# Performance work log

Hardware: AMD Instinct MI355X
Metric: run time of the kernel (lower is better)

Reference implementation:

```python
import jax, jax.numpy as jnp
import numpy as np

D_MODEL = 1024
N_HEADS = 16
D_K = D_MODEL // N_HEADS
B, T = 4, 2048


def setup_inputs() -> dict:
    key = jax.random.key(0)
    ks = jax.random.split(key, 6)
    scale = 1.0 / np.sqrt(D_MODEL)
    q = jax.random.normal(ks[0], (B, T, D_MODEL), dtype=jnp.float32)
    # causal mask: True = masked / ignored (upper triangle)
    causal = jnp.triu(jnp.ones((T, T), dtype=bool), k=1)
    mask = jnp.broadcast_to(causal, (B, 1, T, T))
    Wq = jax.random.normal(ks[1], (D_MODEL, D_MODEL), dtype=jnp.float32) * scale
    Wk = jax.random.normal(ks[2], (D_MODEL, D_MODEL), dtype=jnp.float32) * scale
    Wv = jax.random.normal(ks[3], (D_MODEL, D_MODEL), dtype=jnp.float32) * scale
    Wo = jax.random.normal(ks[4], (D_MODEL, D_MODEL), dtype=jnp.float32) * scale
    bq = jnp.zeros((D_MODEL,), jnp.float32)
    bk = jnp.zeros((D_MODEL,), jnp.float32)
    bv = jnp.zeros((D_MODEL,), jnp.float32)
    bo = jnp.zeros((D_MODEL,), jnp.float32)
    return {"q": q, "mask": mask, "Wq": Wq, "bq": bq, "Wk": Wk, "bk": bk,
            "Wv": Wv, "bv": bv, "Wo": Wo, "bo": bo}


def reference(q, mask, Wq, bq, Wk, bk, Wv, bv, Wo, bo):
    # Self-attention: k = v = q (module defaults). Weights stored torch-style
    # (out, in): y = x @ W.T + b.
    b, tq, _ = q.shape
    qh = (q @ Wq.T + bq).reshape(b, tq, N_HEADS, D_K).transpose(0, 2, 1, 3)  # (B,H,T,dk)
    kh = (q @ Wk.T + bk).reshape(b, tq, N_HEADS, D_K).transpose(0, 2, 1, 3)
    vh = (q @ Wv.T + bv).reshape(b, tq, N_HEADS, D_K).transpose(0, 2, 1, 3)
    attn = jnp.einsum('bhqd,bhkd->bhqk', qh, kh) / np.sqrt(D_K).astype(np.float32)
    attn = jnp.where(mask, -jnp.inf, attn)
    attn = jax.nn.softmax(attn, axis=-1)
    out = jnp.einsum('bhqk,bhkd->bhqd', attn, vh)
    out = out.transpose(0, 2, 1, 3).reshape(b, tq, D_MODEL)
    return out @ Wo.T + bo
```

## Files before the change

### kernel.cpp

```cpp
#include <hip/hip_runtime.h>
#include <hip/hip_bf16.h>
#include <stdint.h>

#define D_MODEL 1024
#define NH      16
#define DKH     64
#define BATCH   4
#define SEQ     2048
#define MROWS   (BATCH*SEQ)

typedef __hip_bfloat16 bf16;
typedef __attribute__((ext_vector_type(8))) short  bf16x8;
typedef __attribute__((ext_vector_type(4))) short  bf16x4;
typedef __attribute__((ext_vector_type(4))) float  f32x4;
typedef __attribute__((ext_vector_type(2))) unsigned int u32x2;

#define CEXP 0.18033688011112042f

__device__ __forceinline__ bf16 f2bf(float x){ return __float2bfloat16(x); }

__device__ __forceinline__ void gload_lds16(const void* g, void* l) {
  __builtin_amdgcn_global_load_lds(
      (const __attribute__((address_space(1))) unsigned int*)g,
      (__attribute__((address_space(3))) unsigned int*)l, 16, 0, 0);
}

__device__ __forceinline__ unsigned int cvtpk(float lo, float hi) {
  unsigned int r;
  asm("v_cvt_pk_bf16_f32 %0, %1, %2" : "=v"(r) : "v"(lo), "v"(hi));
  return r;
}

__global__ __launch_bounds__(256)
void cvt_all(const float* __restrict__ q,
             const float* __restrict__ w0, const float* __restrict__ w1,
             const float* __restrict__ w2, const float* __restrict__ w3,
             bf16* __restrict__ qdst, bf16* __restrict__ wdst)
{
  const int NQB = (MROWS * D_MODEL) / 1024;
  const int bid = blockIdx.x;
  const float* src;
  bf16* dst;
  int i;
  if (bid < NQB) {
    src = q; dst = qdst;
    i = bid * 1024 + threadIdx.x * 4;
  } else {
    const int b2 = bid - NQB;
    const int w = b2 >> 10;
    src = (w == 0) ? w0 : (w == 1) ? w1 : (w == 2) ? w2 : w3;
    dst = wdst + (size_t)w * (D_MODEL * D_MODEL);
    i = (b2 & 1023) * 1024 + threadIdx.x * 4;
  }
  f32x4 v = *(const f32x4*)&src[i];
  union { bf16 e[4]; bf16x4 v4; } u;
  u.e[0] = f2bf(v[0]); u.e[1] = f2bf(v[1]);
  u.e[2] = f2bf(v[2]); u.e[3] = f2bf(v[3]);
  *(bf16x4*)&dst[i] = u.v4;
}

template <int MODE>
__global__ __launch_bounds__(512, 2)
void gemm8(const bf16* __restrict__ A, const bf16* __restrict__ W,
           const float* __restrict__ b0, const float* __restrict__ b1,
           const float* __restrict__ b2, void* __restrict__ Cbase)
{
  constexpr int K    = D_MODEL;
  constexpr int NT   = K / 64;
  constexpr int SLOT = (128 + 256) * 64;
  __shared__ __align__(16) short ring[3 * SLOT];

  const int tid  = threadIdx.x;
  const int lane = tid & 63;
  const int wave = tid >> 6;
  const int lm   = lane & 15;
  const int quad = lane >> 4;
  const int wm   = (wave >> 2) * 64;
  const int wn   = (wave & 3) * 64;
  const int bm   = blockIdx.x * 128;
  const int bn   = blockIdx.y * 256;

  const int rr    = tid >> 3;
  const int kperm = ((tid & 7) ^ (rr & 7)) * 8;
  const bf16* aS0 = A + (int64_t)(bm + rr) * K + kperm;
  const bf16* aS1 = aS0 + (int64_t)64 * K;
  const bf16* bS0 = W + (int64_t)(bn + rr) * K + kperm;
  const bf16* bS1 = bS0 + (int64_t)64 * K;
  const bf16* bS2 = bS0 + (int64_t)128 * K;
  const bf16* bS3 = bS0 + (int64_t)192 * K;

  f32x4 acc[4][4] = {};

#define STAGE8(T, S)                                                          \
  do {                                                                        \
    const int k0_ = (T) * 64;                                                 \
    short* As_ = &ring[(S) * SLOT];                                           \
    short* Bs_ = As_ + 128 * 64;                                              \
    gload_lds16(aS0 + k0_, &As_[tid * 8]);                                    \
    gload_lds16(aS1 + k0_, &As_[(tid + 512) * 8]);                            \
    gload_lds16(bS0 + k0_, &Bs_[tid * 8]);                                    \
    gload_lds16(bS1 + k0_, &Bs_[(tid + 512) * 8]);                            \
    gload_lds16(bS2 + k0_, &Bs_[(tid + 1024) * 8]);                           \
    gload_lds16(bS3 + k0_, &Bs_[(tid + 1536) * 8]);                           \
  } while (0)

  STAGE8(0, 0);
  STAGE8(1, 1);

#pragma unroll
  for (int t = 0; t < NT; ++t) {
    if (t < NT - 1) asm volatile("s_waitcnt vmcnt(6)" ::: "memory");
    else            asm volatile("s_waitcnt vmcnt(0)" ::: "memory");
    __builtin_amdgcn_s_barrier();
    asm volatile("" ::: "memory");

    const short* As = &ring[(t % 3) * SLOT];
    const short* Bs = As + 128 * 64;
    short* Ad = &ring[((t + 2) % 3) * SLOT];
    short* Bd = Ad + 128 * 64;
    const bool dost = (t + 2 < NT);
    const int k2 = (t + 2) * 64;

#pragma unroll
    for (int kk = 0; kk < 2; ++kk) {
      bf16x8 af[4], bfr[4];
#pragma unroll
      for (int i = 0; i < 4; ++i) {
        const int ra = wm + i * 16 + lm;
        af[i]  = *(const bf16x8*)&As[ra * 64 + (((kk * 4 + quad) ^ (ra & 7))) * 8];
        const int rb = wn + i * 16 + lm;
        bfr[i] = *(const bf16x8*)&Bs[rb * 64 + (((kk * 4 + quad) ^ (rb & 7))) * 8];
      }
      if (dost) {
        if (kk == 0) {
          gload_lds16(aS0 + k2, &Ad[tid * 8]);
          gload_lds16(aS1 + k2, &Ad[(tid + 512) * 8]);
          gload_lds16(bS0 + k2, &Bd[tid * 8]);
        } else {
          gload_lds16(bS1 + k2, &Bd[(tid + 512) * 8]);
          gload_lds16(bS2 + k2, &Bd[(tid + 1024) * 8]);
          gload_lds16(bS3 + k2, &Bd[(tid + 1536) * 8]);
        }
      }
      __builtin_amdgcn_s_barrier();
      asm volatile("s_waitcnt lgkmcnt(0)" ::: "memory");
      __builtin_amdgcn_sched_barrier(0);
      __builtin_amdgcn_s_setprio(1);
#pragma unroll
      for (int i = 0; i < 4; ++i)
#pragma unroll
        for (int j = 0; j < 4; ++j)
          acc[i][j] = __builtin_amdgcn_mfma_f32_16x16x32_bf16(af[i], bfr[j], acc[i][j], 0, 0, 0);
      __builtin_amdgcn_s_setprio(0);
    }
  }
#undef STAGE8

  if constexpr (MODE == 1) {
    float* Cp = (float*)Cbase;
#pragma unroll
    for (int j = 0; j < 4; ++j) {
      const int n = bn + wn + j * 16 + lm;
      const float bv = b0[n];
#pragma unroll
      for (int i = 0; i < 4; ++i)
#pragma unroll
        for (int r = 0; r < 4; ++r) {
          const int m = bm + wm + i * 16 + quad * 4 + r;
          Cp[(int64_t)m * D_MODEL + n] = acc[i][j][r] + bv;
        }
    }
  } else {
    const int proj = bn >> 10;
    const int nl0  = bn & 1023;
    const float* bias = (proj == 0) ? b0 : (proj == 1) ? b1 : b2;
    if (proj == 2) {
      bf16* Vt = (bf16*)Cbase + 2 * (size_t)MROWS * D_MODEL;
#pragma unroll
      for (int j = 0; j < 4; ++j) {
        const int nl = nl0 + wn + j * 16 + lm;
        const float bv = bias[nl];
#pragma unroll
        for (int i = 0; i < 4; ++i) {
          const int m0 = bm + wm + i * 16 + quad * 4;
          const int t0 = m0 & 2047;
          const int j64 = t0 & 63;
          const int pos = (((j64 >> 5) * 4 + ((j64 >> 2) & 3)) << 3)
                        + (((j64 >> 4) & 1) << 2);
          const int64_t base = (int64_t)((m0 >> 11) * 16 + (nl >> 6)) * (DKH * SEQ)
                             + (nl & 63) * SEQ + (t0 & ~63) + pos;
          union { bf16 e[4]; bf16x4 v4; } u;
#pragma unroll
          for (int r = 0; r < 4; ++r) u.e[r] = f2bf(acc[i][j][r] + bv);
          *(bf16x4*)&Vt[base] = u.v4;
        }
      }
    } else {
      bf16* Cp = (bf16*)Cbase + (size_t)proj * MROWS * D_MODEL;
      const float sc = (proj == 0) ? CEXP : 1.0f;
#pragma unroll
      for (int j = 0; j < 4; ++j) {
        const int nl = nl0 + wn + j * 16 + lm;
        const float bv = bias[nl];
#pragma unroll
        for (int i = 0; i < 4; ++i)
#pragma unroll
          for (int r = 0; r < 4; ++r) {
            const int m = bm + wm + i * 16 + quad * 4 + r;
            Cp[(int64_t)m * D_MODEL + nl] = f2bf((acc[i][j][r] + bv) * sc);
          }
      }
    }
  }
}

__global__ __launch_bounds__(256)
void attn_causal(const bf16* __restrict__ Q, const bf16* __restrict__ Kg,
                 const bf16* __restrict__ Vt, bf16* __restrict__ O)
{
  __shared__ __align__(16) short lK[2][64 * 64];
  __shared__ __align__(16) short lV[2][64 * 64];

  const int bid  = blockIdx.x;
  const int qt2  = 15 - (bid >> 6);
  const int bh   = bid & 63;

  const int tid  = threadIdx.x;
  const int lane = tid & 63;
  const int wave = tid >> 6;
  const int lm   = lane & 15;
  const int quad = lane >> 4;
  const int qbase = qt2 * 128;
  const int ktmax = 2 * qt2 + 1;
  const int64_t qkbase = (int64_t)((bh >> 4) * SEQ) * D_MODEL + (bh & 15) * DKH;
  const bf16* Kbase = Kg + qkbase;
  const bf16* Vbase = Vt + (int64_t)bh * DKH * SEQ;

  bf16x8 qf[2][2];
#pragma unroll
  for (int g = 0; g < 2; ++g) {
    const bf16* qrow = Q + qkbase
        + (int64_t)(qbase + g * 64 + wave * 16 + lm) * D_MODEL;
    qf[g][0] = *(const bf16x8*)&qrow[quad * 8];
    qf[g][1] = *(const bf16x8*)&qrow[32 + quad * 8];
  }

  f32x4 o_acc[2][4] = {};
  f32x4 o_sum[2]   = {};
  const bf16x8 ones8 = {16256, 16256, 16256, 16256,
                        16256, 16256, 16256, 16256};

  const int srow = tid >> 3;
  const int sg   = (tid & 7) ^ (srow & 7);

  const bf16* kp0 = Kbase + (int64_t)srow        * D_MODEL + sg * 8;
  const bf16* kp1 = Kbase + (int64_t)(srow + 32) * D_MODEL + sg * 8;
  const bf16* vp0 = Vbase + (int64_t)srow        * SEQ + sg * 8;
  const bf16* vp1 = Vbase + (int64_t)(srow + 32) * SEQ + sg * 8;

#define STAGE(KB, BUF)                                                        \
  do {                                                                        \
    gload_lds16(kp0 + (int64_t)(KB) * D_MODEL, &lK[BUF][tid * 8]);            \
    gload_lds16(kp1 + (int64_t)(KB) * D_MODEL, &lK[BUF][(tid + 256) * 8]);    \
    gload_lds16(vp0 + (KB), &lV[BUF][tid * 8]);                               \
    gload_lds16(vp1 + (KB), &lV[BUF][(tid + 256) * 8]);                       \
  } while (0)

  STAGE(0, 0);

  for (int kt = 0; kt <= ktmax; ++kt) {
    const int cur = kt & 1;
    __syncthreads();
    if (kt < ktmax) STAGE((kt + 1) * 64, cur ^ 1);

    const short* lKc = lK[cur];
    const short* lVc = lV[cur];

    f32x4 s[2][4];
    __builtin_amdgcn_s_setprio(1);
#pragma unroll
    for (int ni = 0; ni < 4; ++ni) {
      const int row = ni * 16 + lm;
      const bf16x8 k0 = *(const bf16x8*)&lKc[row * 64 + ((quad       ^ (row & 7))) * 8];
      const bf16x8 k1 = *(const bf16x8*)&lKc[row * 64 + (((4 + quad) ^ (row & 7))) * 8];
#pragma unroll
      for (int g = 0; g < 2; ++g) {
        f32x4 zz = {};
        zz = __builtin_amdgcn_mfma_f32_16x16x32_bf16(k0, qf[g][0], zz, 0, 0, 0);
        zz = __builtin_amdgcn_mfma_f32_16x16x32_bf16(k1, qf[g][1], zz, 0, 0, 0);
        s[g][ni] = zz;
      }
    }
    __builtin_amdgcn_s_setprio(0);

#pragma unroll
    for (int g = 0; g < 2; ++g) {
      if (kt >= 2 * qt2 + g) {
        const int qv = qbase + g * 64 + wave * 16 + lm;
        const int kb = kt * 64;
#pragma unroll
        for (int ni = 0; ni < 4; ++ni) {
          const int kp_ = kb + ni * 16 + quad * 4;
#pragma unroll
          for (int r = 0; r < 4; ++r)
            if (kp_ + r > qv) s[g][ni][r] = -1e30f;
        }
      }
    }

    unsigned int pku[2][4][2];
#pragma unroll
    for (int g = 0; g < 2; ++g)
#pragma unroll
      for (int ni = 0; ni < 4; ++ni) {
        pku[g][ni][0] = cvtpk(__builtin_amdgcn_exp2f(s[g][ni][0]),
                              __builtin_amdgcn_exp2f(s[g][ni][1]));
        pku[g][ni][1] = cvtpk(__builtin_amdgcn_exp2f(s[g][ni][2]),
                              __builtin_amdgcn_exp2f(s[g][ni][3]));
      }

    __builtin_amdgcn_s_setprio(1);
#pragma unroll
    for (int m = 0; m < 2; ++m) {
      union { unsigned int u[4]; bf16x8 v; } au[2];
#pragma unroll
      for (int g = 0; g < 2; ++g) {
        au[g].u[0] = pku[g][2 * m][0];     au[g].u[1] = pku[g][2 * m][1];
        au[g].u[2] = pku[g][2 * m + 1][0]; au[g].u[3] = pku[g][2 * m + 1][1];
        o_sum[g] = __builtin_amdgcn_mfma_f32_16x16x32_bf16(au[g].v, ones8, o_sum[g], 0, 0, 0);
      }
#pragma unroll
      for (int di = 0; di < 4; ++di) {
        const int vrow = di * 16 + lm;
        const bf16x8 vb = *(const bf16x8*)&lVc[vrow * 64
            + (((m * 4 + quad) ^ (vrow & 7))) * 8];
#pragma unroll
        for (int g = 0; g < 2; ++g)
          o_acc[g][di] = __builtin_amdgcn_mfma_f32_16x16x32_bf16(au[g].v, vb, o_acc[g][di], 0, 0, 0);
      }
    }
    __builtin_amdgcn_s_setprio(0);
  }
#undef STAGE

#pragma unroll
  for (int g = 0; g < 2; ++g) {
    float lr[4];
#pragma unroll
    for (int r = 0; r < 4; ++r) lr[r] = 1.0f / o_sum[g][r];
#pragma unroll
    for (int di = 0; di < 4; ++di)
#pragma unroll
      for (int r = 0; r < 4; ++r) {
        const int qrow = qbase + g * 64 + wave * 16 + quad * 4 + r;
        O[qkbase + (int64_t)qrow * D_MODEL + di * 16 + lm]
            = f2bf(o_acc[g][di][r] * lr[r]);
      }
  }
}

extern "C" void kernel_launch(void* const* d_in, const int* in_sizes, int n_in,
                              void* d_out, int out_size, void* d_ws, size_t ws_size,
                              hipStream_t stream)
{
  const float* q  = (const float*)d_in[0];
  const float* Wq = (const float*)d_in[2];
  const float* bq = (const float*)d_in[3];
  const float* Wk = (const float*)d_in[4];
  const float* bk = (const float*)d_in[5];
  const float* Wv = (const float*)d_in[6];
  const float* bv = (const float*)d_in[7];
  const float* Wo = (const float*)d_in[8];
  const float* bo = (const float*)d_in[9];
  float* out = (float*)d_out;

  const size_t NQ = (size_t)MROWS * D_MODEL;
  const size_t NW = (size_t)D_MODEL * D_MODEL;

  bf16* qb  = (bf16*)d_ws;
  bf16* Wb  = qb + NQ;
  bf16* Qw  = Wb + 4 * NW;
  bf16* Kw  = Qw + NQ;
  bf16* Vtw = Kw + NQ;

  cvt_all<<<dim3(NQ / 1024 + 4 * NW / 1024), 256, 0, stream>>>(
      q, Wq, Wk, Wv, Wo, qb, Wb);

  gemm8<0><<<dim3(MROWS / 128, 3 * D_MODEL / 256), 512, 0, stream>>>(
      qb, Wb, bq, bk, bv, Qw);

  attn_causal<<<dim3(BATCH * NH * (SEQ / 128)), 256, 0, stream>>>(Qw, Kw, Vtw, qb);

  gemm8<1><<<dim3(MROWS / 128, D_MODEL / 256), 512, 0, stream>>>(
      qb, Wb + 3 * NW, bo, bo, bo, out);
}
```

Before: 277.2 us.

## Shrink attention q-tile to 64 rows with 2-wave blocks

The attention kernel now handles 64 query rows per block with 128 threads (2 waves of 32 rows each) instead of 128 rows with 4 waves, which doubles the grid to 2048 blocks. Each block loops only up to its own diagonal tile, so the causal masked waste on the diagonal shrinks and load balance across CUs is finer. The trade-off is that each K/V tile staged in LDS is reused by half as many query rows, so staging traffic per unit of compute roughly doubles, and each thread now issues more global-to-LDS loads.

```diff
diff --git a/kernel.cpp b/kernel.cpp
--- a/kernel.cpp
+++ b/kernel.cpp
@@ -214,7 +214,7 @@
   }
 }
 
-__global__ __launch_bounds__(256)
+__global__ __launch_bounds__(128)
 void attn_causal(const bf16* __restrict__ Q, const bf16* __restrict__ Kg,
                  const bf16* __restrict__ Vt, bf16* __restrict__ O)
 {
@@ -222,7 +222,7 @@
   __shared__ __align__(16) short lV[2][64 * 64];
 
   const int bid  = blockIdx.x;
-  const int qt2  = 15 - (bid >> 6);
+  const int qt   = 31 - (bid >> 6);
   const int bh   = bid & 63;
 
   const int tid  = threadIdx.x;
@@ -230,8 +230,7 @@
   const int wave = tid >> 6;
   const int lm   = lane & 15;
   const int quad = lane >> 4;
-  const int qbase = qt2 * 128;
-  const int ktmax = 2 * qt2 + 1;
+  const int qbase = qt * 64;
   const int64_t qkbase = (int64_t)((bh >> 4) * SEQ) * D_MODEL + (bh & 15) * DKH;
   const bf16* Kbase = Kg + qkbase;
   const bf16* Vbase = Vt + (int64_t)bh * DKH * SEQ;
@@ -240,7 +239,7 @@
 #pragma unroll
   for (int g = 0; g < 2; ++g) {
     const bf16* qrow = Q + qkbase
-        + (int64_t)(qbase + g * 64 + wave * 16 + lm) * D_MODEL;
+        + (int64_t)(qbase + wave * 32 + g * 16 + lm) * D_MODEL;
     qf[g][0] = *(const bf16x8*)&qrow[quad * 8];
     qf[g][1] = *(const bf16x8*)&qrow[32 + quad * 8];
   }
@@ -253,25 +252,26 @@
   const int srow = tid >> 3;
   const int sg   = (tid & 7) ^ (srow & 7);
 
-  const bf16* kp0 = Kbase + (int64_t)srow        * D_MODEL + sg * 8;
-  const bf16* kp1 = Kbase + (int64_t)(srow + 32) * D_MODEL + sg * 8;
-  const bf16* vp0 = Vbase + (int64_t)srow        * SEQ + sg * 8;
-  const bf16* vp1 = Vbase + (int64_t)(srow + 32) * SEQ + sg * 8;
+  const bf16* kp = Kbase + (int64_t)srow * D_MODEL + sg * 8;
+  const bf16* vp = Vbase + (int64_t)srow * SEQ + sg * 8;
 
 #define STAGE(KB, BUF)                                                        \
   do {                                                                        \
-    gload_lds16(kp0 + (int64_t)(KB) * D_MODEL, &lK[BUF][tid * 8]);            \
-    gload_lds16(kp1 + (int64_t)(KB) * D_MODEL, &lK[BUF][(tid + 256) * 8]);    \
-    gload_lds16(vp0 + (KB), &lV[BUF][tid * 8]);                               \
-    gload_lds16(vp1 + (KB), &lV[BUF][(tid + 256) * 8]);                       \
+    _Pragma("unroll")                                                         \
+    for (int p = 0; p < 4; ++p) {                                             \
+      gload_lds16(kp + (int64_t)((KB) + 16 * p) * D_MODEL,                    \
+                  &lK[BUF][(tid + 128 * p) * 8]);                             \
+      gload_lds16(vp + (KB) + 16 * p * SEQ,                                   \
+                  &lV[BUF][(tid + 128 * p) * 8]);                             \
+    }                                                                         \
   } while (0)
 
   STAGE(0, 0);
 
-  for (int kt = 0; kt <= ktmax; ++kt) {
+  for (int kt = 0; kt <= qt; ++kt) {
     const int cur = kt & 1;
     __syncthreads();
-    if (kt < ktmax) STAGE((kt + 1) * 64, cur ^ 1);
+    if (kt < qt) STAGE((kt + 1) * 64, cur ^ 1);
 
     const short* lKc = lK[cur];
     const short* lVc = lV[cur];
@@ -293,14 +293,13 @@
     }
     __builtin_amdgcn_s_setprio(0);
 
-#pragma unroll
-    for (int g = 0; g < 2; ++g) {
-      if (kt >= 2 * qt2 + g) {
-        const int qv = qbase + g * 64 + wave * 16 + lm;
-        const int kb = kt * 64;
+    if (kt == qt) {
+#pragma unroll
+      for (int g = 0; g < 2; ++g) {
+        const int qv = qbase + wave * 32 + g * 16 + lm;
 #pragma unroll
         for (int ni = 0; ni < 4; ++ni) {
-          const int kp_ = kb + ni * 16 + quad * 4;
+          const int kp_ = qbase + ni * 16 + quad * 4;
 #pragma unroll
           for (int r = 0; r < 4; ++r)
             if (kp_ + r > qv) s[g][ni][r] = -1e30f;
@@ -352,7 +351,7 @@
     for (int di = 0; di < 4; ++di)
 #pragma unroll
       for (int r = 0; r < 4; ++r) {
-        const int qrow = qbase + g * 64 + wave * 16 + quad * 4 + r;
+        const int qrow = qbase + wave * 32 + g * 16 + quad * 4 + r;
         O[qkbase + (int64_t)qrow * D_MODEL + di * 16 + lm]
             = f2bf(o_acc[g][di][r] * lr[r]);
       }
@@ -389,7 +388,7 @@
   gemm8<0><<<dim3(MROWS / 128, 3 * D_MODEL / 256), 512, 0, stream>>>(
       qb, Wb, bq, bk, bv, Qw);
 
-  attn_causal<<<dim3(BATCH * NH * (SEQ / 128)), 256, 0, stream>>>(Qw, Kw, Vtw, qb);
+  attn_causal<<<dim3(BATCH * NH * (SEQ / 64)), 128, 0, stream>>>(Qw, Kw, Vtw, qb);
 
   gemm8<1><<<dim3(MROWS / 128, D_MODEL / 256), 512, 0, stream>>>(
       qb, Wb + 3 * NW, bo, bo, bo, out);
```

Result: faster. 269.8 us (-2.7%).
